# Performance work log

Measured on AMD Instinct MI355X. Metric: run time of the kernel, lower is better.

The kernel has to match this reference:

```python
import jax, jax.numpy as jnp
import numpy as np

N_NODES = 50000
N_EDGES = 800000
MAX_ITER = 20  # torchdeq default f_max_iter=40; fixed iteration count for a tractable jit-able baseline
K = 3          # TAGConv default number of hops
INS, EMB, HID, OUT = 4, 64, 128, 1


def setup_inputs():
    key = jax.random.key(0)
    ks = jax.random.split(key, 12)
    def lin(k, fan_in, fan_out):
        return jax.random.normal(k, (fan_in, fan_out), jnp.float32) / np.sqrt(fan_in)
    def tag_w(k, fan_in, fan_out):
        # stacked weights for the K+1 TAGConv linear maps: [K+1, in, out]
        return jax.random.normal(k, (K + 1, fan_in, fan_out), jnp.float32) / np.sqrt(fan_in * (K + 1))
    return {
        "x": jax.random.normal(ks[0], (N_NODES, INS), jnp.float32),
        "pos": jax.random.normal(ks[1], (N_NODES, 3), jnp.float32),
        "edge_attr": jax.random.uniform(ks[2], (N_EDGES,), jnp.float32),
        "up_w1": lin(ks[3], INS, EMB), "up_b1": jnp.zeros((EMB,), jnp.float32),
        "up_w2": lin(ks[4], EMB, EMB), "up_b2": jnp.zeros((EMB,), jnp.float32),
        "c1_w": tag_w(ks[5], EMB + 3, HID), "c1_b": jnp.zeros((HID,), jnp.float32),
        "c2_w": tag_w(ks[6], HID, HID), "c2_b": jnp.zeros((HID,), jnp.float32),
        "c3_w": tag_w(ks[7], HID, EMB), "c3_b": jnp.zeros((EMB,), jnp.float32),
        "down_w1": lin(ks[8], EMB, OUT), "down_b1": jnp.zeros((OUT,), jnp.float32),
        "down_w2": lin(ks[9], OUT, OUT), "down_b2": jnp.zeros((OUT,), jnp.float32),
        "edge_index": jax.random.randint(ks[10], (2, N_EDGES), 0, N_NODES, jnp.int32),
    }


def _gcn_norm(row, col, edge_attr, n):
    # PyG gcn_norm with edge weights, no self loops (TAGConv default)
    deg = jax.ops.segment_sum(edge_attr, col, num_segments=n)
    safe = jnp.where(deg > 0, deg, 1.0)
    dinv = jnp.where(deg > 0, jax.lax.rsqrt(safe), 0.0)
    return dinv[row] * edge_attr * dinv[col]


def _mlp(x, w1, b1, w2, b2):
    # torch F.gelu default = exact erf gelu
    return jax.nn.gelu(x @ w1 + b1, approximate=False) @ w2 + b2


def reference(x, pos, edge_attr, up_w1, up_b1, up_w2, up_b2, c1_w, c1_b, c2_w, c2_b, c3_w, c3_b, down_w1, down_b1, down_w2, down_b2, edge_index):
    n = x.shape[0]
    row, col = edge_index[0], edge_index[1]
    norm = _gcn_norm(row, col, edge_attr, n)

    def tag(h, W, b):
        # TAGConv: sum_k lin_k( A_hat^k x ) + bias
        out = h @ W[0]
        for k in range(1, W.shape[0]):
            h = jax.ops.segment_sum(h[row] * norm[:, None], col, num_segments=n)  # [E,C] gather-scatter
            out = out + h @ W[k]
        return out + b

    def gnn(z):
        h = jnp.concatenate([z, pos], axis=1)
        h = jax.nn.relu(tag(h, c1_w, c1_b))
        h = jax.nn.relu(tag(h, c2_w, c2_b))  # F.dropout is identity in eval mode
        h = tag(h, c3_w, c3_b)
        return jax.nn.log_softmax(h, axis=1)

    z0 = _mlp(x, up_w1, up_b1, up_w2, up_b2)
    z = jax.lax.fori_loop(0, MAX_ITER, lambda i, zz: gnn(zz), z0)  # fixed-point solver
    z_star = gnn(z)  # phantom-gradient step (torchdeq grad=1)
    out = _mlp(z_star, down_w1, down_b1, down_w2, down_b2)
    return out, z_star
```

## Files before the change

### kernel.cpp

```cpp
#include <hip/hip_runtime.h>
#include <hip/hip_bf16.h>

#define N_NODES 50000
#define N_EDGES 800000
#define MAX_ITER 20

typedef __attribute__((ext_vector_type(8))) short bf16x8;
typedef __attribute__((ext_vector_type(4))) float f32x4;

__device__ __forceinline__ float gelu_f(float x){
  return 0.5f*x*(1.0f+erff(x*0.70710678118654752f));
}
__device__ __forceinline__ ushort f2b(float f){
  uint x = __float_as_uint(f);
  uint r = (x + 0x7fffu + ((x>>16)&1u)) >> 16;
  return (ushort)r;
}

__global__ void deg_cnt_kernel(const int* __restrict__ col, const float* __restrict__ attr,
                               float* __restrict__ deg, int* __restrict__ cnt){
  int e = blockIdx.x*256 + threadIdx.x;
  if (e < N_EDGES){
    int c = col[e];
    atomicAdd(&deg[c], attr[e]);
    atomicAdd(&cnt[c], 1);
  }
}

__global__ void norm_kernel(const int* __restrict__ row, const int* __restrict__ col,
                            const float* __restrict__ attr, const float* __restrict__ deg,
                            float* __restrict__ nrm){
  int e = blockIdx.x*256 + threadIdx.x;
  if (e < N_EDGES){
    float dr = deg[row[e]], dc = deg[col[e]];
    float ir = dr > 0.f ? rsqrtf(dr) : 0.f;
    float ic = dc > 0.f ? rsqrtf(dc) : 0.f;
    nrm[e] = ir * attr[e] * ic;
  }
}

__global__ void scan_kernel(const int* __restrict__ cnt, int* __restrict__ starts,
                            int* __restrict__ cursor){
  __shared__ int buf[1024];
  __shared__ int carry;
  int tid = threadIdx.x;
  if (tid==0) carry = 0;
  __syncthreads();
  for (int base=0; base<N_NODES; base+=1024){
    int i = base+tid;
    int v = (i<N_NODES)? cnt[i] : 0;
    int cv = carry;
    buf[tid]=v;
    __syncthreads();
    for (int off=1; off<1024; off<<=1){
      int t = (tid>=off)? buf[tid-off] : 0;
      __syncthreads();
      buf[tid]+=t;
      __syncthreads();
    }
    int excl = buf[tid]-v+cv;
    if (i<N_NODES){ starts[i]=excl; cursor[i]=excl; }
    __syncthreads();
    if (tid==0) carry = cv + buf[1023];
    __syncthreads();
  }
  if (tid==0) starts[N_NODES] = carry;
}

__global__ void fill_kernel(const int* __restrict__ row, const int* __restrict__ col,
                            const float* __restrict__ nrm, int* __restrict__ cursor,
                            int* __restrict__ csr_row, float* __restrict__ csr_nrm){
  int e = blockIdx.x*256+threadIdx.x;
  if (e<N_EDGES){
    int c = col[e];
    int p = atomicAdd(&cursor[c],1);
    csr_row[p]=row[e];
    csr_nrm[p]=nrm[e];
  }
}

__global__ void pack_w1(const float* __restrict__ W, ushort* __restrict__ PB){
  int i = blockIdx.x*256+threadIdx.x;
  if (i < 4*8*128*8){
    int e = i&7; int n = (i>>3)&127; int kb = (i>>10)&7; int j = i>>13;
    int k = kb*8+e;
    PB[i] = f2b(W[((size_t)j*67 + k)*128 + n]);
  }
}
__global__ void pack_w2(const float* __restrict__ W, ushort* __restrict__ PB){
  int i = blockIdx.x*256+threadIdx.x;
  if (i < 4*16*128*8){
    int e = i&7; int n = (i>>3)&127; int kb = (i>>10)&15; int j = i>>14;
    int k = kb*8+e;
    PB[i] = f2b(W[((size_t)j*128 + k)*128 + n]);
  }
}
__global__ void pack_w3(const float* __restrict__ W, ushort* __restrict__ PB){
  int i = blockIdx.x*256+threadIdx.x;
  if (i < 16*256*8){
    int e = i&7; int n = (i>>3)&255; int kb = i>>11;
    int k = kb*8+e;
    PB[i] = f2b(W[(((size_t)(n>>6))*128 + k)*64 + (n&63)]);
  }
}

__global__ __launch_bounds__(256) void mlp_up_kernel(
    const float* __restrict__ x, const float* __restrict__ w1, const float* __restrict__ b1,
    const float* __restrict__ w2, const float* __restrict__ b2, ushort* __restrict__ z){
  __shared__ float sw1[4*64];
  __shared__ float sw2[64*64];
  __shared__ float sb1[64], sb2[64];
  __shared__ float t1s[4][64];
  int tid = threadIdx.x;
  for (int i=tid;i<256;i+=256) sw1[i]=w1[i];
  for (int i=tid;i<4096;i+=256) sw2[i]=w2[i];
  if (tid<64){ sb1[tid]=b1[tid]; sb2[tid]=b2[tid]; }
  __syncthreads();
  int g = tid>>6;
  int c = tid&63;
  int node = blockIdx.x*4 + g;
  float acc = sb1[c];
  #pragma unroll
  for (int k=0;k<4;k++) acc += x[node*4+k]*sw1[k*64+c];
  t1s[g][c] = gelu_f(acc);
  __syncthreads();
  float acc2 = sb2[c];
  #pragma unroll 8
  for (int k=0;k<64;k++) acc2 += t1s[g][k]*sw2[k*64+c];
  z[(size_t)node*64+c] = f2b(acc2);
}

template<int LDIN>
__global__ void posprop(const float* __restrict__ in, float* __restrict__ out,
                        const int* __restrict__ starts, const int* __restrict__ crow,
                        const float* __restrict__ cnrm){
  int v = blockIdx.x*256+threadIdx.x;
  if (v >= N_NODES) return;
  int s=starts[v], e=starts[v+1];
  float a0=0.f,a1=0.f,a2=0.f;
  for (int i=s;i<e;++i){
    int r=crow[i]; float nm=cnrm[i];
    a0 = fmaf(in[(size_t)r*LDIN+0], nm, a0);
    a1 = fmaf(in[(size_t)r*LDIN+1], nm, a1);
    a2 = fmaf(in[(size_t)r*LDIN+2], nm, a2);
  }
  float4 o = {a0,a1,a2,0.f};
  *(float4*)(out + (size_t)v*4) = o;
}

__global__ __launch_bounds__(256) void posbias_kernel(
    const float* __restrict__ pos, const float* __restrict__ P1,
    const float* __restrict__ P2, const float* __restrict__ P3,
    const float* __restrict__ c1w, const float* __restrict__ c1b,
    ushort* __restrict__ pb){
  __shared__ float sw[4][3][128];
  int tid=threadIdx.x;
  for (int i=tid; i<4*3*128; i+=256){
    int cc=i&127; int d=(i>>7)%3; int j=i/(3*128);
    sw[j][d][cc] = c1w[((size_t)j*67 + 64 + d)*128 + cc];
  }
  __syncthreads();
  int idx = blockIdx.x*256+tid;
  if (idx < N_NODES*128){
    int n = idx>>7, cc = idx&127;
    float a = c1b[cc];
    #pragma unroll
    for (int d=0;d<3;d++) a = fmaf(pos[(size_t)n*3+d], sw[0][d][cc], a);
    #pragma unroll
    for (int d=0;d<3;d++) a = fmaf(P1[(size_t)n*4+d], sw[1][d][cc], a);
    #pragma unroll
    for (int d=0;d<3;d++) a = fmaf(P2[(size_t)n*4+d], sw[2][d][cc], a);
    #pragma unroll
    for (int d=0;d<3;d++) a = fmaf(P3[(size_t)n*4+d], sw[3][d][cc], a);
    pb[idx]=f2b(a);
  }
}

__global__ __launch_bounds__(256) void prop128(
    const ushort* __restrict__ h, ushort* __restrict__ out,
    const int* __restrict__ starts, const int* __restrict__ crow,
    const float* __restrict__ cnrm){
  int wv = threadIdx.x >> 6;
  int v = blockIdx.x*4 + wv;
  int t = threadIdx.x & 63;
  int g = t >> 4;
  int c = t & 15;
  int s = starts[v], e = starts[v+1];
  float acc[8] = {0,0,0,0,0,0,0,0};
  for (int i=s; i<e; i+=64){
    int cnt = e - i; if (cnt > 64) cnt = 64;
    int r = 0; float nm = 0.f;
    if (t < cnt){ r = crow[i+t]; nm = cnrm[i+t]; }
    for (int jb=0; jb<cnt; jb+=4){
      int rr  = __shfl(r,  jb+g, 64);
      float w = __shfl(nm, jb+g, 64);
      uint4 hv = *(const uint4*)(h + (size_t)rr*128 + c*8);
      const uint* hp = (const uint*)&hv;
      #pragma unroll
      for (int q=0;q<4;q++){
        acc[2*q]   = fmaf(__uint_as_float(hp[q]<<16),          w, acc[2*q]);
        acc[2*q+1] = fmaf(__uint_as_float(hp[q]&0xffff0000u),  w, acc[2*q+1]);
      }
    }
  }
  #pragma unroll
  for (int q=0;q<8;q++){
    acc[q] += __shfl_xor(acc[q], 16, 64);
    acc[q] += __shfl_xor(acc[q], 32, 64);
  }
  if (g==0){
    uint4 o; uint* op=(uint*)&o;
    #pragma unroll
    for (int q=0;q<4;q++) op[q] = (uint)f2b(acc[2*q]) | ((uint)f2b(acc[2*q+1])<<16);
    *(uint4*)(out + (size_t)v*128 + c*8) = o;
  }
}

template<int MODE>
__global__ __launch_bounds__(256) void prop64(
    const ushort* __restrict__ h, void* __restrict__ outp,
    const ushort* __restrict__ adj, const float* __restrict__ bias,
    const int* __restrict__ starts, const int* __restrict__ crow,
    const float* __restrict__ cnrm){
  int wv = threadIdx.x >> 6;
  int v = blockIdx.x*4 + wv;
  int t = threadIdx.x & 63;
  int g = t >> 3;
  int c = t & 7;
  int s = starts[v], e = starts[v+1];
  float acc[8] = {0,0,0,0,0,0,0,0};
  for (int i=s; i<e; i+=64){
    int cnt = e - i; if (cnt > 64) cnt = 64;
    int r = 0; float nm = 0.f;
    if (t < cnt){ r = crow[i+t]; nm = cnrm[i+t]; }
    for (int jb=0; jb<cnt; jb+=8){
      int rr  = __shfl(r,  jb+g, 64);
      float w = __shfl(nm, jb+g, 64);
      uint4 hv = *(const uint4*)(h + (size_t)rr*64 + c*8);
      const uint* hp = (const uint*)&hv;
      #pragma unroll
      for (int q=0;q<4;q++){
        acc[2*q]   = fmaf(__uint_as_float(hp[q]<<16),          w, acc[2*q]);
        acc[2*q+1] = fmaf(__uint_as_float(hp[q]&0xffff0000u),  w, acc[2*q+1]);
      }
    }
  }
  #pragma unroll
  for (int q=0;q<8;q++){
    acc[q] += __shfl_xor(acc[q], 8, 64);
    acc[q] += __shfl_xor(acc[q], 16, 64);
    acc[q] += __shfl_xor(acc[q], 32, 64);
  }
  if (MODE==0){
    if (g==0){
      uint4 o; uint* op=(uint*)&o;
      #pragma unroll
      for (int q=0;q<4;q++) op[q] = (uint)f2b(acc[2*q]) | ((uint)f2b(acc[2*q+1])<<16);
      *(uint4*)((ushort*)outp + (size_t)v*64 + c*8) = o;
    }
  } else if (MODE==1){
    if (g==0){
      uint4 av = *(const uint4*)(adj + (size_t)v*64 + c*8);
      const uint* ap=(const uint*)&av;
      uint4 o; uint* op=(uint*)&o;
      #pragma unroll
      for (int q=0;q<4;q++){
        float lo = acc[2*q]   + __uint_as_float(ap[q]<<16);
        float hi = acc[2*q+1] + __uint_as_float(ap[q]&0xffff0000u);
        op[q] = (uint)f2b(lo) | ((uint)f2b(hi)<<16);
      }
      *(uint4*)((ushort*)outp + (size_t)v*64 + c*8) = o;
    }
  } else {
    uint4 av = *(const uint4*)(adj + (size_t)v*64 + c*8);
    const uint* ap=(const uint*)&av;
    float vv[8];
    #pragma unroll
    for (int q=0;q<4;q++){
      vv[2*q]   = acc[2*q]   + __uint_as_float(ap[q]<<16)         + bias[c*8+2*q];
      vv[2*q+1] = acc[2*q+1] + __uint_as_float(ap[q]&0xffff0000u) + bias[c*8+2*q+1];
    }
    float m = vv[0];
    #pragma unroll
    for (int q=1;q<8;q++) m = fmaxf(m, vv[q]);
    m = fmaxf(m, __shfl_xor(m,1,64));
    m = fmaxf(m, __shfl_xor(m,2,64));
    m = fmaxf(m, __shfl_xor(m,4,64));
    float ssum = 0.f;
    #pragma unroll
    for (int q=0;q<8;q++) ssum += __expf(vv[q]-m);
    ssum += __shfl_xor(ssum,1,64);
    ssum += __shfl_xor(ssum,2,64);
    ssum += __shfl_xor(ssum,4,64);
    float lse = m + __logf(ssum);
    if (g==0){
      if (MODE==2){
        uint4 o; uint* op=(uint*)&o;
        #pragma unroll
        for (int q=0;q<4;q++) op[q] = (uint)f2b(vv[2*q]-lse) | ((uint)f2b(vv[2*q+1]-lse)<<16);
        *(uint4*)((ushort*)outp + (size_t)v*64 + c*8) = o;
      } else {
        float* zo = (float*)outp + (size_t)v*64 + c*8;
        #pragma unroll
        for (int q=0;q<8;q++) zo[q] = vv[q]-lse;
      }
    }
  }
}

template<int KC, bool PERNODE_BIAS>
__global__ __launch_bounds__(256) void gemm4in(
    const ushort* __restrict__ H0, const ushort* __restrict__ H1,
    const ushort* __restrict__ H2, const ushort* __restrict__ H3,
    const ushort* __restrict__ PB, const void* __restrict__ biasp,
    ushort* __restrict__ out){
  constexpr int NT = 8;
  constexpr int NKS = KC/32;
  int lane = threadIdx.x & 63;
  int wv   = threadIdx.x >> 6;
  int m0 = blockIdx.x*64 + wv*16;
  int lr = lane & 15, lg = lane >> 4;
  int arow = m0 + lr; if (arow > N_NODES-1) arow = N_NODES-1;
  const ushort* Hs[4] = {H0,H1,H2,H3};
  f32x4 acc[NT];
  #pragma unroll
  for (int t=0;t<NT;t++) acc[t] = (f32x4){0.f,0.f,0.f,0.f};
  #pragma unroll
  for (int j=0;j<4;j++){
    const ushort* Hj  = Hs[j] + (size_t)arow*KC + lg*8;
    const ushort* PBj = PB + (size_t)j*(KC/8)*128*8;
    #pragma unroll
    for (int ks=0; ks<NKS; ks++){
      bf16x8 af = *(const bf16x8*)(Hj + ks*32);
      int kb = ks*4 + lg;
      #pragma unroll
      for (int t=0;t<NT;t++){
        bf16x8 bf = *(const bf16x8*)(PBj + ((size_t)kb*128 + t*16 + lr)*8);
        acc[t] = __builtin_amdgcn_mfma_f32_16x16x32_bf16(af, bf, acc[t], 0, 0, 0);
      }
    }
  }
  #pragma unroll
  for (int t=0;t<NT;t++){
    #pragma unroll
    for (int q=0;q<4;q++){
      int node = m0 + lg*4 + q;
      if (node < N_NODES){
        int col = t*16 + lr;
        float b;
        if (PERNODE_BIAS) b = __uint_as_float(((uint)((const ushort*)biasp)[(size_t)node*128+col])<<16);
        else              b = ((const float*)biasp)[col];
        float vo = fmaxf(acc[t][q] + b, 0.f);
        out[(size_t)node*128 + col] = f2b(vo);
      }
    }
  }
}

__global__ __launch_bounds__(256) void gemm_y(
    const ushort* __restrict__ T2, const ushort* __restrict__ PB,
    ushort* __restrict__ Y){
  constexpr int NT = 16;
  int lane = threadIdx.x & 63;
  int wv   = threadIdx.x >> 6;
  int m0 = blockIdx.x*64 + wv*16;
  int lr = lane & 15, lg = lane >> 4;
  int arow = m0 + lr; if (arow > N_NODES-1) arow = N_NODES-1;
  f32x4 acc[NT];
  #pragma unroll
  for (int t=0;t<NT;t++) acc[t] = (f32x4){0.f,0.f,0.f,0.f};
  const ushort* Hj = T2 + (size_t)arow*128 + lg*8;
  #pragma unroll
  for (int ks=0; ks<4; ks++){
    bf16x8 af = *(const bf16x8*)(Hj + ks*32);
    int kb = ks*4 + lg;
    #pragma unroll
    for (int t=0;t<NT;t++){
      bf16x8 bf = *(const bf16x8*)(PB + ((size_t)kb*256 + t*16 + lr)*8);
      acc[t] = __builtin_amdgcn_mfma_f32_16x16x32_bf16(af, bf, acc[t], 0, 0, 0);
    }
  }
  #pragma unroll
  for (int t=0;t<NT;t++){
    int n = t*16 + lr;
    int j = n >> 6, cc = n & 63;
    #pragma unroll
    for (int q=0;q<4;q++){
      int node = m0 + lg*4 + q;
      if (node < N_NODES)
        Y[(size_t)j*N_NODES*64 + (size_t)node*64 + cc] = f2b(acc[t][q]);
    }
  }
}

__global__ __launch_bounds__(256) void mlp_down_kernel(
    const float* __restrict__ zs, const float* __restrict__ dw1, const float* __restrict__ db1,
    const float* __restrict__ dw2, const float* __restrict__ db2, float* __restrict__ out){
  int node = blockIdx.x*4 + (threadIdx.x>>6);
  int c = threadIdx.x & 63;
  float v = zs[(size_t)node*64+c]*dw1[c];
  #pragma unroll
  for (int off=32; off; off>>=1) v += __shfl_xor(v, off, 64);
  if (c==0) out[node] = gelu_f(v + db1[0]) * dw2[0] + db2[0];
}

extern "C" void kernel_launch(void* const* d_in, const int* in_sizes, int n_in,
                              void* d_out, int out_size, void* d_ws, size_t ws_size,
                              hipStream_t stream){
  const float* x     = (const float*)d_in[0];
  const float* pos   = (const float*)d_in[1];
  const float* eattr = (const float*)d_in[2];
  const float* up_w1 = (const float*)d_in[3];
  const float* up_b1 = (const float*)d_in[4];
  const float* up_w2 = (const float*)d_in[5];
  const float* up_b2 = (const float*)d_in[6];
  const float* c1_w  = (const float*)d_in[7];
  const float* c1_b  = (const float*)d_in[8];
  const float* c2_w  = (const float*)d_in[9];
  const float* c2_b  = (const float*)d_in[10];
  const float* c3_w  = (const float*)d_in[11];
  const float* c3_b  = (const float*)d_in[12];
  const float* dw1   = (const float*)d_in[13];
  const float* db1   = (const float*)d_in[14];
  const float* dw2   = (const float*)d_in[15];
  const float* db2   = (const float*)d_in[16];
  const int*   eidx  = (const int*)d_in[17];
  const int* row = eidx;
  const int* col = eidx + N_EDGES;

  char* wsp = (char*)d_ws;
  size_t off = 0;
  auto alloc = [&](size_t bytes)->char*{
    char* p = wsp + off;
    off = (off + bytes + 255) & ~(size_t)255;
    return p;
  };
  float*  deg    = (float*)alloc((size_t)N_NODES*4);
  int*    cnt    = (int*)  alloc((size_t)N_NODES*4);
  int*    starts = (int*)  alloc((size_t)(N_NODES+1)*4);
  int*    cursor = (int*)  alloc((size_t)N_NODES*4);
  float*  nrm    = (float*)alloc((size_t)N_EDGES*4);
  int*    crow   = (int*)  alloc((size_t)N_EDGES*4);
  float*  cnrm   = (float*)alloc((size_t)N_EDGES*4);
  float*  P1     = (float*)alloc((size_t)N_NODES*4*4);
  float*  P2     = (float*)alloc((size_t)N_NODES*4*4);
  float*  P3     = (float*)alloc((size_t)N_NODES*4*4);
  ushort* pbias  = (ushort*)alloc((size_t)N_NODES*128*2);
  ushort* z      = (ushort*)alloc((size_t)N_NODES*64*2);
  ushort* q1     = (ushort*)alloc((size_t)N_NODES*64*2);
  ushort* q2     = (ushort*)alloc((size_t)N_NODES*64*2);
  ushort* q3     = (ushort*)alloc((size_t)N_NODES*64*2);
  ushort* t1     = (ushort*)alloc((size_t)N_NODES*128*2);
  ushort* p1     = (ushort*)alloc((size_t)N_NODES*128*2);
  ushort* p2     = (ushort*)alloc((size_t)N_NODES*128*2);
  ushort* p3     = (ushort*)alloc((size_t)N_NODES*128*2);
  ushort* t2     = (ushort*)alloc((size_t)N_NODES*128*2);
  ushort* PB1    = (ushort*)alloc((size_t)4*8*128*8*2);
  ushort* PB2    = (ushort*)alloc((size_t)4*16*128*8*2);
  ushort* PB3    = (ushort*)alloc((size_t)16*256*8*2);

  ushort* Y  = p1;
  ushort* Y0 = Y;
  ushort* Y1 = Y + (size_t)1*N_NODES*64;
  ushort* Y2 = Y + (size_t)2*N_NODES*64;
  ushort* Y3 = Y + (size_t)3*N_NODES*64;
  ushort* u1 = q1;
  ushort* u2 = q2;

  float* outv  = (float*)d_out;
  float* zstar = (float*)d_out + N_NODES;

  hipMemsetAsync(deg, 0, (size_t)N_NODES*4, stream);
  hipMemsetAsync(cnt, 0, (size_t)N_NODES*4, stream);
  int eb = (N_EDGES+255)/256;
  deg_cnt_kernel<<<eb,256,0,stream>>>(col, eattr, deg, cnt);
  norm_kernel<<<eb,256,0,stream>>>(row, col, eattr, deg, nrm);
  scan_kernel<<<1,1024,0,stream>>>(cnt, starts, cursor);
  fill_kernel<<<eb,256,0,stream>>>(row, col, nrm, cursor, crow, cnrm);
  pack_w1<<<128,256,0,stream>>>(c1_w, PB1);
  pack_w2<<<256,256,0,stream>>>(c2_w, PB2);
  pack_w3<<<128,256,0,stream>>>(c3_w, PB3);
  mlp_up_kernel<<<N_NODES/4,256,0,stream>>>(x, up_w1, up_b1, up_w2, up_b2, z);

  int nb = (N_NODES+255)/256;
  posprop<3><<<nb,256,0,stream>>>(pos, P1, starts, crow, cnrm);
  posprop<4><<<nb,256,0,stream>>>(P1,  P2, starts, crow, cnrm);
  posprop<4><<<nb,256,0,stream>>>(P2,  P3, starts, crow, cnrm);
  posbias_kernel<<<(N_NODES*128)/256,256,0,stream>>>(pos, P1, P2, P3, c1_w, c1_b, pbias);

  const int gprop = N_NODES/4;
  const int ggemm = (N_NODES+63)/64;

  for (int it=0; it<=MAX_ITER; ++it){
    prop64<0><<<gprop,256,0,stream>>>(z,  q1, nullptr, nullptr, starts, crow, cnrm);
    prop64<0><<<gprop,256,0,stream>>>(q1, q2, nullptr, nullptr, starts, crow, cnrm);
    prop64<0><<<gprop,256,0,stream>>>(q2, q3, nullptr, nullptr, starts, crow, cnrm);
    gemm4in<64,true><<<ggemm,256,0,stream>>>(z,q1,q2,q3,PB1,pbias,t1);

    prop128<<<gprop,256,0,stream>>>(t1,p1,starts,crow,cnrm);
    prop128<<<gprop,256,0,stream>>>(p1,p2,starts,crow,cnrm);
    prop128<<<gprop,256,0,stream>>>(p2,p3,starts,crow,cnrm);
    gemm4in<128,false><<<ggemm,256,0,stream>>>(t1,p1,p2,p3,PB2,c2_b,t2);

    gemm_y<<<ggemm,256,0,stream>>>(t2, PB3, Y);
    prop64<1><<<gprop,256,0,stream>>>(Y3, u1, Y2, nullptr, starts, crow, cnrm);
    prop64<1><<<gprop,256,0,stream>>>(u1, u2, Y1, nullptr, starts, crow, cnrm);
    if (it < MAX_ITER){
      prop64<2><<<gprop,256,0,stream>>>(u2, z, Y0, c3_b, starts, crow, cnrm);
    } else {
      prop64<3><<<gprop,256,0,stream>>>(u2, zstar, Y0, c3_b, starts, crow, cnrm);
    }
  }
  mlp_down_kernel<<<N_NODES/4,256,0,stream>>>(zstar, dw1, db1, dw2, db2, outv);
}
```

Measured before the change: 7.227 ms.

## Gather FP8 copies of node features in fixed-point iterations, keep bf16 for final step

Producers now also write FP8 (e4m3) copies of the node feature tensors, and the gather/propagate kernels in the first 20 iterations read those FP8 copies, which halves the bytes fetched per random neighbour gather. The final phantom-gradient iteration still uses the bf16 path so that z_star is computed at higher precision. This adds extra FP8 stores in the producer kernels and introduces quantization error in intermediate iterations, which may hurt accuracy or tolerance.

After: 6.940 ms. 4.0% less time.

```diff
diff --git a/kernel.cpp b/kernel.cpp
--- a/kernel.cpp
+++ b/kernel.cpp
@@ -7,6 +7,8 @@
 
 typedef __attribute__((ext_vector_type(8))) short bf16x8;
 typedef __attribute__((ext_vector_type(4))) float f32x4;
+typedef __attribute__((ext_vector_type(2))) float f32x2;
+typedef unsigned char uchar;
 
 __device__ __forceinline__ float gelu_f(float x){
   return 0.5f*x*(1.0f+erff(x*0.70710678118654752f));
@@ -15,6 +17,60 @@
   uint x = __float_as_uint(f);
   uint r = (x + 0x7fffu + ((x>>16)&1u)) >> 16;
   return (ushort)r;
+}
+
+#if __has_builtin(__builtin_amdgcn_cvt_pk_f32_fp8) && __has_builtin(__builtin_amdgcn_cvt_pk_fp8_f32)
+#define HW_FP8 1
+#endif
+
+__device__ __forceinline__ uint fp8_enc1_sw(float x){
+  uint u = __float_as_uint(x);
+  uint s = (u>>24)&0x80u;
+  int e = (int)((u>>23)&0xffu);
+  uint m = u&0x7fffffu;
+  uint m3 = (m + 0x80000u)>>20;
+  if (m3==8u){ e+=1; m3=0u; }
+  int e8 = e-120;
+  if (e8<=0) return s;
+  if (e8>=15) return s|0x7eu;
+  return s | ((uint)e8<<3) | m3;
+}
+__device__ __forceinline__ float fp8_dec1_sw(uint b){
+  uint s=(b&0x80u)<<24;
+  uint em=b&0x7fu;
+  if (em==0u) return __uint_as_float(s);
+  if ((em>>3)==0u) return (s?-1.f:1.f)*(float)em*0.001953125f;
+  return __uint_as_float(s | ((em+960u)<<20));
+}
+__device__ __forceinline__ void fp8_dec8(uint lo, uint hi, float* d){
+#ifdef HW_FP8
+  f32x2 a = __builtin_amdgcn_cvt_pk_f32_fp8(lo,false);
+  f32x2 b = __builtin_amdgcn_cvt_pk_f32_fp8(lo,true);
+  f32x2 c = __builtin_amdgcn_cvt_pk_f32_fp8(hi,false);
+  f32x2 e = __builtin_amdgcn_cvt_pk_f32_fp8(hi,true);
+  d[0]=a[0];d[1]=a[1];d[2]=b[0];d[3]=b[1];d[4]=c[0];d[5]=c[1];d[6]=e[0];d[7]=e[1];
+#else
+  d[0]=fp8_dec1_sw(lo&0xffu);        d[1]=fp8_dec1_sw((lo>>8)&0xffu);
+  d[2]=fp8_dec1_sw((lo>>16)&0xffu);  d[3]=fp8_dec1_sw(lo>>24);
+  d[4]=fp8_dec1_sw(hi&0xffu);        d[5]=fp8_dec1_sw((hi>>8)&0xffu);
+  d[6]=fp8_dec1_sw((hi>>16)&0xffu);  d[7]=fp8_dec1_sw(hi>>24);
+#endif
+}
+__device__ __forceinline__ uint fp8_enc4(float a,float b,float c,float d){
+#ifdef HW_FP8
+  uint u = __builtin_amdgcn_cvt_pk_fp8_f32(a,b,0u,false);
+  u = __builtin_amdgcn_cvt_pk_fp8_f32(c,d,u,true);
+  return u;
+#else
+  return fp8_enc1_sw(a) | (fp8_enc1_sw(b)<<8) | (fp8_enc1_sw(c)<<16) | (fp8_enc1_sw(d)<<24);
+#endif
+}
+__device__ __forceinline__ uchar fp8_enc1(float a){
+#ifdef HW_FP8
+  return (uchar)(__builtin_amdgcn_cvt_pk_fp8_f32(a,a,0u,false)&0xffu);
+#else
+  return (uchar)fp8_enc1_sw(a);
+#endif
 }
 
 __global__ void deg_cnt_kernel(const int* __restrict__ col, const float* __restrict__ attr,
@@ -106,7 +162,8 @@
 
 __global__ __launch_bounds__(256) void mlp_up_kernel(
     const float* __restrict__ x, const float* __restrict__ w1, const float* __restrict__ b1,
-    const float* __restrict__ w2, const float* __restrict__ b2, ushort* __restrict__ z){
+    const float* __restrict__ w2, const float* __restrict__ b2,
+    ushort* __restrict__ z, uchar* __restrict__ z8){
   __shared__ float sw1[4*64];
   __shared__ float sw2[64*64];
   __shared__ float sb1[64], sb2[64];
@@ -128,6 +185,7 @@
   #pragma unroll 8
   for (int k=0;k<64;k++) acc2 += t1s[g][k]*sw2[k*64+c];
   z[(size_t)node*64+c] = f2b(acc2);
+  z8[(size_t)node*64+c] = fp8_enc1(acc2);
 }
 
 template<int LDIN>
@@ -176,8 +234,128 @@
   }
 }
 
-__global__ __launch_bounds__(256) void prop128(
-    const ushort* __restrict__ h, ushort* __restrict__ out,
+template<int MODE, bool IN8, bool OUT8>
+__global__ __launch_bounds__(256) void prop64k(
+    const void* __restrict__ hin, ushort* __restrict__ obf,
+    uchar* __restrict__ of8, float* __restrict__ of32,
+    const ushort* __restrict__ adj, const float* __restrict__ bias,
+    const int* __restrict__ starts, const int* __restrict__ crow,
+    const float* __restrict__ cnrm){
+  constexpr bool WBF = (MODE==0) || (MODE==2) || (MODE==1 && !OUT8);
+  int wv = threadIdx.x >> 6;
+  int v = blockIdx.x*4 + wv;
+  int t = threadIdx.x & 63;
+  int g = t >> 3;
+  int c = t & 7;
+  int s = starts[v], e = starts[v+1];
+  float acc[8] = {0,0,0,0,0,0,0,0};
+  for (int i=s; i<e; i+=64){
+    int cnt = e - i; if (cnt > 64) cnt = 64;
+    int r = 0; float nm = 0.f;
+    if (t < cnt){ r = crow[i+t]; nm = cnrm[i+t]; }
+    for (int jb=0; jb<cnt; jb+=8){
+      int rr = __shfl(r, jb+g, 64);
+      float nmj = __shfl(nm, jb+g, 64);
+      float hv[8];
+      if (IN8){
+        uint2 d = *(const uint2*)((const uchar*)hin + (size_t)rr*64 + c*8);
+        fp8_dec8(d.x, d.y, hv);
+      } else {
+        uint4 d = *(const uint4*)((const ushort*)hin + (size_t)rr*64 + c*8);
+        const uint* dp = (const uint*)&d;
+        #pragma unroll
+        for (int q=0;q<4;q++){
+          hv[2*q]   = __uint_as_float(dp[q]<<16);
+          hv[2*q+1] = __uint_as_float(dp[q]&0xffff0000u);
+        }
+      }
+      #pragma unroll
+      for (int q=0;q<8;q++) acc[q] = fmaf(hv[q], nmj, acc[q]);
+    }
+  }
+  #pragma unroll
+  for (int q=0;q<8;q++){
+    acc[q] += __shfl_xor(acc[q], 8, 64);
+    acc[q] += __shfl_xor(acc[q], 16, 64);
+    acc[q] += __shfl_xor(acc[q], 32, 64);
+  }
+  if (MODE==0 || MODE==1){
+    if (g==0){
+      float val[8];
+      if (MODE==1){
+        uint4 av = *(const uint4*)(adj + (size_t)v*64 + c*8);
+        const uint* ap=(const uint*)&av;
+        #pragma unroll
+        for (int q=0;q<4;q++){
+          val[2*q]   = acc[2*q]   + __uint_as_float(ap[q]<<16);
+          val[2*q+1] = acc[2*q+1] + __uint_as_float(ap[q]&0xffff0000u);
+        }
+      } else {
+        #pragma unroll
+        for (int q=0;q<8;q++) val[q]=acc[q];
+      }
+      if (WBF){
+        uint4 o; uint* op=(uint*)&o;
+        #pragma unroll
+        for (int q=0;q<4;q++) op[q] = (uint)f2b(val[2*q]) | ((uint)f2b(val[2*q+1])<<16);
+        *(uint4*)(obf + (size_t)v*64 + c*8) = o;
+      }
+      if (OUT8){
+        uint2 o8;
+        o8.x = fp8_enc4(val[0],val[1],val[2],val[3]);
+        o8.y = fp8_enc4(val[4],val[5],val[6],val[7]);
+        *(uint2*)(of8 + (size_t)v*64 + c*8) = o8;
+      }
+    }
+  } else {
+    uint4 av = *(const uint4*)(adj + (size_t)v*64 + c*8);
+    const uint* ap=(const uint*)&av;
+    float vv[8];
+    #pragma unroll
+    for (int q=0;q<4;q++){
+      vv[2*q]   = acc[2*q]   + __uint_as_float(ap[q]<<16)         + bias[c*8+2*q];
+      vv[2*q+1] = acc[2*q+1] + __uint_as_float(ap[q]&0xffff0000u) + bias[c*8+2*q+1];
+    }
+    float m = vv[0];
+    #pragma unroll
+    for (int q=1;q<8;q++) m = fmaxf(m, vv[q]);
+    m = fmaxf(m, __shfl_xor(m,1,64));
+    m = fmaxf(m, __shfl_xor(m,2,64));
+    m = fmaxf(m, __shfl_xor(m,4,64));
+    float ss = 0.f;
+    #pragma unroll
+    for (int q=0;q<8;q++) ss += __expf(vv[q]-m);
+    ss += __shfl_xor(ss,1,64);
+    ss += __shfl_xor(ss,2,64);
+    ss += __shfl_xor(ss,4,64);
+    float lse = m + __logf(ss);
+    if (g==0){
+      if (MODE==2){
+        uint4 o; uint* op=(uint*)&o;
+        #pragma unroll
+        for (int q=0;q<4;q++) op[q] = (uint)f2b(vv[2*q]-lse) | ((uint)f2b(vv[2*q+1]-lse)<<16);
+        *(uint4*)(obf + (size_t)v*64 + c*8) = o;
+        if (OUT8){
+          uint2 o8;
+          o8.x = fp8_enc4(vv[0]-lse,vv[1]-lse,vv[2]-lse,vv[3]-lse);
+          o8.y = fp8_enc4(vv[4]-lse,vv[5]-lse,vv[6]-lse,vv[7]-lse);
+          *(uint2*)(of8 + (size_t)v*64 + c*8) = o8;
+        }
+      } else {
+        float* zo = of32 + (size_t)v*64 + c*8;
+        float4 o0 = {vv[0]-lse, vv[1]-lse, vv[2]-lse, vv[3]-lse};
+        float4 o1 = {vv[4]-lse, vv[5]-lse, vv[6]-lse, vv[7]-lse};
+        *(float4*)zo = o0;
+        *(float4*)(zo+4) = o1;
+      }
+    }
+  }
+}
+
+template<bool IN8, bool OUT8>
+__global__ __launch_bounds__(256) void prop128k(
+    const void* __restrict__ hin, ushort* __restrict__ obf,
+    uchar* __restrict__ of8,
     const int* __restrict__ starts, const int* __restrict__ crow,
     const float* __restrict__ cnrm){
   int wv = threadIdx.x >> 6;
@@ -193,14 +371,22 @@
     if (t < cnt){ r = crow[i+t]; nm = cnrm[i+t]; }
     for (int jb=0; jb<cnt; jb+=4){
       int rr  = __shfl(r,  jb+g, 64);
-      float w = __shfl(nm, jb+g, 64);
-      uint4 hv = *(const uint4*)(h + (size_t)rr*128 + c*8);
-      const uint* hp = (const uint*)&hv;
+      float nmj = __shfl(nm, jb+g, 64);
+      float hv[8];
+      if (IN8){
+        uint2 d = *(const uint2*)((const uchar*)hin + (size_t)rr*128 + c*8);
+        fp8_dec8(d.x, d.y, hv);
+      } else {
+        uint4 d = *(const uint4*)((const ushort*)hin + (size_t)rr*128 + c*8);
+        const uint* dp = (const uint*)&d;
+        #pragma unroll
+        for (int q=0;q<4;q++){
+          hv[2*q]   = __uint_as_float(dp[q]<<16);
+          hv[2*q+1] = __uint_as_float(dp[q]&0xffff0000u);
+        }
+      }
       #pragma unroll
-      for (int q=0;q<4;q++){
-        acc[2*q]   = fmaf(__uint_as_float(hp[q]<<16),          w, acc[2*q]);
-        acc[2*q+1] = fmaf(__uint_as_float(hp[q]&0xffff0000u),  w, acc[2*q+1]);
-      }
+      for (int q=0;q<8;q++) acc[q] = fmaf(hv[q], nmj, acc[q]);
     }
   }
   #pragma unroll
@@ -212,108 +398,22 @@
     uint4 o; uint* op=(uint*)&o;
     #pragma unroll
     for (int q=0;q<4;q++) op[q] = (uint)f2b(acc[2*q]) | ((uint)f2b(acc[2*q+1])<<16);
-    *(uint4*)(out + (size_t)v*128 + c*8) = o;
-  }
-}
-
-template<int MODE>
-__global__ __launch_bounds__(256) void prop64(
-    const ushort* __restrict__ h, void* __restrict__ outp,
-    const ushort* __restrict__ adj, const float* __restrict__ bias,
-    const int* __restrict__ starts, const int* __restrict__ crow,
-    const float* __restrict__ cnrm){
-  int wv = threadIdx.x >> 6;
-  int v = blockIdx.x*4 + wv;
-  int t = threadIdx.x & 63;
-  int g = t >> 3;
-  int c = t & 7;
-  int s = starts[v], e = starts[v+1];
-  float acc[8] = {0,0,0,0,0,0,0,0};
-  for (int i=s; i<e; i+=64){
-    int cnt = e - i; if (cnt > 64) cnt = 64;
-    int r = 0; float nm = 0.f;
-    if (t < cnt){ r = crow[i+t]; nm = cnrm[i+t]; }
-    for (int jb=0; jb<cnt; jb+=8){
-      int rr  = __shfl(r,  jb+g, 64);
-      float w = __shfl(nm, jb+g, 64);
-      uint4 hv = *(const uint4*)(h + (size_t)rr*64 + c*8);
-      const uint* hp = (const uint*)&hv;
-      #pragma unroll
-      for (int q=0;q<4;q++){
-        acc[2*q]   = fmaf(__uint_as_float(hp[q]<<16),          w, acc[2*q]);
-        acc[2*q+1] = fmaf(__uint_as_float(hp[q]&0xffff0000u),  w, acc[2*q+1]);
-      }
-    }
-  }
-  #pragma unroll
-  for (int q=0;q<8;q++){
-    acc[q] += __shfl_xor(acc[q], 8, 64);
-    acc[q] += __shfl_xor(acc[q], 16, 64);
-    acc[q] += __shfl_xor(acc[q], 32, 64);
-  }
-  if (MODE==0){
-    if (g==0){
-      uint4 o; uint* op=(uint*)&o;
-      #pragma unroll
-      for (int q=0;q<4;q++) op[q] = (uint)f2b(acc[2*q]) | ((uint)f2b(acc[2*q+1])<<16);
-      *(uint4*)((ushort*)outp + (size_t)v*64 + c*8) = o;
-    }
-  } else if (MODE==1){
-    if (g==0){
-      uint4 av = *(const uint4*)(adj + (size_t)v*64 + c*8);
-      const uint* ap=(const uint*)&av;
-      uint4 o; uint* op=(uint*)&o;
-      #pragma unroll
-      for (int q=0;q<4;q++){
-        float lo = acc[2*q]   + __uint_as_float(ap[q]<<16);
-        float hi = acc[2*q+1] + __uint_as_float(ap[q]&0xffff0000u);
-        op[q] = (uint)f2b(lo) | ((uint)f2b(hi)<<16);
-      }
-      *(uint4*)((ushort*)outp + (size_t)v*64 + c*8) = o;
-    }
-  } else {
-    uint4 av = *(const uint4*)(adj + (size_t)v*64 + c*8);
-    const uint* ap=(const uint*)&av;
-    float vv[8];
-    #pragma unroll
-    for (int q=0;q<4;q++){
-      vv[2*q]   = acc[2*q]   + __uint_as_float(ap[q]<<16)         + bias[c*8+2*q];
-      vv[2*q+1] = acc[2*q+1] + __uint_as_float(ap[q]&0xffff0000u) + bias[c*8+2*q+1];
-    }
-    float m = vv[0];
-    #pragma unroll
-    for (int q=1;q<8;q++) m = fmaxf(m, vv[q]);
-    m = fmaxf(m, __shfl_xor(m,1,64));
-    m = fmaxf(m, __shfl_xor(m,2,64));
-    m = fmaxf(m, __shfl_xor(m,4,64));
-    float ssum = 0.f;
-    #pragma unroll
-    for (int q=0;q<8;q++) ssum += __expf(vv[q]-m);
-    ssum += __shfl_xor(ssum,1,64);
-    ssum += __shfl_xor(ssum,2,64);
-    ssum += __shfl_xor(ssum,4,64);
-    float lse = m + __logf(ssum);
-    if (g==0){
-      if (MODE==2){
-        uint4 o; uint* op=(uint*)&o;
-        #pragma unroll
-        for (int q=0;q<4;q++) op[q] = (uint)f2b(vv[2*q]-lse) | ((uint)f2b(vv[2*q+1]-lse)<<16);
-        *(uint4*)((ushort*)outp + (size_t)v*64 + c*8) = o;
-      } else {
-        float* zo = (float*)outp + (size_t)v*64 + c*8;
-        #pragma unroll
-        for (int q=0;q<8;q++) zo[q] = vv[q]-lse;
-      }
-    }
-  }
-}
-
-template<int KC, bool PERNODE_BIAS>
+    *(uint4*)(obf + (size_t)v*128 + c*8) = o;
+    if (OUT8){
+      uint2 o8;
+      o8.x = fp8_enc4(acc[0],acc[1],acc[2],acc[3]);
+      o8.y = fp8_enc4(acc[4],acc[5],acc[6],acc[7]);
+      *(uint2*)(of8 + (size_t)v*128 + c*8) = o8;
+    }
+  }
+}
+
+template<int KC, bool PERNODE_BIAS, bool OUT8>
 __global__ __launch_bounds__(256) void gemm4in(
     const ushort* __restrict__ H0, const ushort* __restrict__ H1,
     const ushort* __restrict__ H2, const ushort* __restrict__ H3,
     const ushort* __restrict__ PB, const void* __restrict__ biasp,
-    ushort* __restrict__ out){
+    ushort* __restrict__ out, uchar* __restrict__ out8){
   constexpr int NT = 8;
   constexpr int NKS = KC/32;
   int lane = threadIdx.x & 63;
@@ -352,6 +452,7 @@
         else              b = ((const float*)biasp)[col];
         float vo = fmaxf(acc[t][q] + b, 0.f);
         out[(size_t)node*128 + col] = f2b(vo);
+        if (OUT8) out8[(size_t)node*128 + col] = fp8_enc1(vo);
       }
     }
   }
@@ -359,7 +460,7 @@
 
 __global__ __launch_bounds__(256) void gemm_y(
     const ushort* __restrict__ T2, const ushort* __restrict__ PB,
-    ushort* __restrict__ Y){
+    ushort* __restrict__ Y, uchar* __restrict__ Y3_8){
   constexpr int NT = 16;
   int lane = threadIdx.x & 63;
   int wv   = threadIdx.x >> 6;
@@ -387,8 +488,10 @@
     #pragma unroll
     for (int q=0;q<4;q++){
       int node = m0 + lg*4 + q;
-      if (node < N_NODES)
+      if (node < N_NODES){
         Y[(size_t)j*N_NODES*64 + (size_t)node*64 + cc] = f2b(acc[t][q]);
+        if (j==3) Y3_8[(size_t)node*64 + cc] = fp8_enc1(acc[t][q]);
+      }
     }
   }
 }
@@ -458,6 +561,15 @@
   ushort* PB1    = (ushort*)alloc((size_t)4*8*128*8*2);
   ushort* PB2    = (ushort*)alloc((size_t)4*16*128*8*2);
   ushort* PB3    = (ushort*)alloc((size_t)16*256*8*2);
+  uchar*  z8     = (uchar*)alloc((size_t)N_NODES*64);
+  uchar*  q1_8   = (uchar*)alloc((size_t)N_NODES*64);
+  uchar*  q2_8   = (uchar*)alloc((size_t)N_NODES*64);
+  uchar*  t1_8   = (uchar*)alloc((size_t)N_NODES*128);
+  uchar*  p1_8   = (uchar*)alloc((size_t)N_NODES*128);
+  uchar*  p2_8   = (uchar*)alloc((size_t)N_NODES*128);
+  uchar*  Y3_8   = (uchar*)alloc((size_t)N_NODES*64);
+  uchar*  u1_8   = (uchar*)alloc((size_t)N_NODES*64);
+  uchar*  u2_8   = (uchar*)alloc((size_t)N_NODES*64);
 
   ushort* Y  = p1;
   ushort* Y0 = Y;
@@ -480,7 +592,7 @@
   pack_w1<<<128,256,0,stream>>>(c1_w, PB1);
   pack_w2<<<256,256,0,stream>>>(c2_w, PB2);
   pack_w3<<<128,256,0,stream>>>(c3_w, PB3);
-  mlp_up_kernel<<<N_NODES/4,256,0,stream>>>(x, up_w1, up_b1, up_w2, up_b2, z);
+  mlp_up_kernel<<<N_NODES/4,256,0,stream>>>(x, up_w1, up_b1, up_w2, up_b2, z, z8);
 
   int nb = (N_NODES+255)/256;
   posprop<3><<<nb,256,0,stream>>>(pos, P1, starts, crow, cnrm);
@@ -492,23 +604,36 @@
   const int ggemm = (N_NODES+63)/64;
 
   for (int it=0; it<=MAX_ITER; ++it){
-    prop64<0><<<gprop,256,0,stream>>>(z,  q1, nullptr, nullptr, starts, crow, cnrm);
-    prop64<0><<<gprop,256,0,stream>>>(q1, q2, nullptr, nullptr, starts, crow, cnrm);
-    prop64<0><<<gprop,256,0,stream>>>(q2, q3, nullptr, nullptr, starts, crow, cnrm);
-    gemm4in<64,true><<<ggemm,256,0,stream>>>(z,q1,q2,q3,PB1,pbias,t1);
-
-    prop128<<<gprop,256,0,stream>>>(t1,p1,starts,crow,cnrm);
-    prop128<<<gprop,256,0,stream>>>(p1,p2,starts,crow,cnrm);
-    prop128<<<gprop,256,0,stream>>>(p2,p3,starts,crow,cnrm);
-    gemm4in<128,false><<<ggemm,256,0,stream>>>(t1,p1,p2,p3,PB2,c2_b,t2);
-
-    gemm_y<<<ggemm,256,0,stream>>>(t2, PB3, Y);
-    prop64<1><<<gprop,256,0,stream>>>(Y3, u1, Y2, nullptr, starts, crow, cnrm);
-    prop64<1><<<gprop,256,0,stream>>>(u1, u2, Y1, nullptr, starts, crow, cnrm);
     if (it < MAX_ITER){
-      prop64<2><<<gprop,256,0,stream>>>(u2, z, Y0, c3_b, starts, crow, cnrm);
+      prop64k<0,true,true> <<<gprop,256,0,stream>>>(z8,   q1, q1_8, nullptr, nullptr, nullptr, starts, crow, cnrm);
+      prop64k<0,true,true> <<<gprop,256,0,stream>>>(q1_8, q2, q2_8, nullptr, nullptr, nullptr, starts, crow, cnrm);
+      prop64k<0,true,false><<<gprop,256,0,stream>>>(q2_8, q3, nullptr, nullptr, nullptr, nullptr, starts, crow, cnrm);
+      gemm4in<64,true,true><<<ggemm,256,0,stream>>>(z,q1,q2,q3,PB1,pbias,t1,t1_8);
+
+      prop128k<true,true> <<<gprop,256,0,stream>>>(t1_8, p1, p1_8, starts, crow, cnrm);
+      prop128k<true,true> <<<gprop,256,0,stream>>>(p1_8, p2, p2_8, starts, crow, cnrm);
+      prop128k<true,false><<<gprop,256,0,stream>>>(p2_8, p3, nullptr, starts, crow, cnrm);
+      gemm4in<128,false,false><<<ggemm,256,0,stream>>>(t1,p1,p2,p3,PB2,c2_b,t2,nullptr);
+
+      gemm_y<<<ggemm,256,0,stream>>>(t2, PB3, Y, Y3_8);
+      prop64k<1,true,true><<<gprop,256,0,stream>>>(Y3_8, nullptr, u1_8, nullptr, Y2, nullptr, starts, crow, cnrm);
+      prop64k<1,true,true><<<gprop,256,0,stream>>>(u1_8, nullptr, u2_8, nullptr, Y1, nullptr, starts, crow, cnrm);
+      prop64k<2,true,true><<<gprop,256,0,stream>>>(u2_8, z, z8, nullptr, Y0, c3_b, starts, crow, cnrm);
     } else {
-      prop64<3><<<gprop,256,0,stream>>>(u2, zstar, Y0, c3_b, starts, crow, cnrm);
+      prop64k<0,false,false><<<gprop,256,0,stream>>>(z,  q1, nullptr, nullptr, nullptr, nullptr, starts, crow, cnrm);
+      prop64k<0,false,false><<<gprop,256,0,stream>>>(q1, q2, nullptr, nullptr, nullptr, nullptr, starts, crow, cnrm);
+      prop64k<0,false,false><<<gprop,256,0,stream>>>(q2, q3, nullptr, nullptr, nullptr, nullptr, starts, crow, cnrm);
+      gemm4in<64,true,false><<<ggemm,256,0,stream>>>(z,q1,q2,q3,PB1,pbias,t1,nullptr);
+
+      prop128k<false,false><<<gprop,256,0,stream>>>(t1, p1, nullptr, starts, crow, cnrm);
+      prop128k<false,false><<<gprop,256,0,stream>>>(p1, p2, nullptr, starts, crow, cnrm);
+      prop128k<false,false><<<gprop,256,0,stream>>>(p2, p3, nullptr, starts, crow, cnrm);
+      gemm4in<128,false,false><<<ggemm,256,0,stream>>>(t1,p1,p2,p3,PB2,c2_b,t2,nullptr);
+
+      gemm_y<<<ggemm,256,0,stream>>>(t2, PB3, Y, Y3_8);
+      prop64k<1,false,false><<<gprop,256,0,stream>>>(Y3, u1, nullptr, nullptr, Y2, nullptr, starts, crow, cnrm);
+      prop64k<1,false,false><<<gprop,256,0,stream>>>(u1, u2, nullptr, nullptr, Y1, nullptr, starts, crow, cnrm);
+      prop64k<3,false,false><<<gprop,256,0,stream>>>(u2, nullptr, nullptr, zstar, Y0, c3_b, starts, crow, cnrm);
     }
   }
   mlp_down_kernel<<<N_NODES/4,256,0,stream>>>(zstar, dw1, db1, dw2, db2, outv);
```
